# Kernel tuning notes

Hardware: AMD Instinct MI355X
Metric: run time of the kernel (lower is better)

## Reference

```python
import jax, jax.numpy as jnp
import numpy as np
import math

HIDDEN = 1024
N_HEADS = 16
N_KV = 4
HEAD_DIM = HIDDEN // N_HEADS  # 64
B, S = 2, 2048
THETA = 100000.0


def _freqs_cos_sin(dim, end, theta):
    # yarn params: original_max_position_embeddings=2048 >= end, so no ramp scaling,
    # attention_factor=1.0 -> plain RoPE frequencies.
    inv = 1.0 / theta ** (np.arange(0, dim, 2)[: dim // 2] / dim)
    t = np.arange(end)
    f = np.outer(t, inv).astype(np.float32)  # (end, dim/2)
    cos = np.concatenate([np.cos(f), np.cos(f)], axis=-1)  # (end, dim)
    sin = np.concatenate([np.sin(f), np.sin(f)], axis=-1)
    return jnp.asarray(cos), jnp.asarray(sin)


def _rotate(x):
    # stack([-x[...,1::2], x[...,::2]], -1).reshape_as(x)
    return jnp.stack([-x[..., 1::2], x[..., ::2]], axis=-1).reshape(x.shape)


def setup_inputs() -> dict:
    key = jax.random.key(0)
    ks = jax.random.split(key, 9)
    s = 0.02
    return {
        "hidden_states": jax.random.normal(ks[0], (B, S, HIDDEN), jnp.float32),
        "attention_mask": jnp.ones((B, S), jnp.int32),
        "Wq": jax.random.normal(ks[1], (HIDDEN, HIDDEN), jnp.float32) * s,
        "bq": jnp.zeros((HIDDEN,), jnp.float32),
        "Wk": jax.random.normal(ks[2], (HIDDEN, N_KV * HEAD_DIM), jnp.float32) * s,
        "bk": jnp.zeros((N_KV * HEAD_DIM,), jnp.float32),
        "Wv": jax.random.normal(ks[3], (HIDDEN, N_KV * HEAD_DIM), jnp.float32) * s,
        "bv": jnp.zeros((N_KV * HEAD_DIM,), jnp.float32),
        "Wo": jax.random.normal(ks[4], (HIDDEN, HIDDEN), jnp.float32) * s,
        "bo": jnp.zeros((HIDDEN,), jnp.float32),
    }


def reference(hidden_states, attention_mask, Wq, bq, Wk, bk, Wv, bv, Wo, bo):
    b, s, _ = hidden_states.shape
    q = (hidden_states @ Wq + bq).reshape(b, s, N_HEADS, HEAD_DIM)
    k = (hidden_states @ Wk + bk).reshape(b, s, N_KV, HEAD_DIM)
    v = (hidden_states @ Wv + bv).reshape(b, s, N_KV, HEAD_DIM)

    cos, sin = _freqs_cos_sin(HEAD_DIM, s, THETA)
    cos = cos[:, None, :]  # (s,1,d) broadcasts over (b,s,h,d)
    sin = sin[:, None, :]
    q = q * cos + _rotate(q) * sin
    k = k * cos + _rotate(k) * sin

    # GQA: repeat_interleave kv heads -> jnp.repeat along head axis
    rep = N_HEADS // N_KV
    k = jnp.repeat(k, rep, axis=2)
    v = jnp.repeat(v, rep, axis=2)

    scores = jnp.einsum("bqhd,bkhd->bhqk", q, k) / math.sqrt(HEAD_DIM)
    neg = jnp.finfo(scores.dtype).min
    causal = jnp.triu(jnp.ones((s, s), bool), k=1)  # (q,kv)
    bias = jnp.where(causal, neg, 0.0).astype(scores.dtype)[None, None]
    key_mask = attention_mask.astype(bool)[:, None, None, :]  # (b,1,1,kv)
    bias = jnp.where(key_mask, bias, neg)
    probs = jax.nn.softmax(scores + bias, axis=-1)
    attn = jnp.einsum("bhqk,bkhd->bqhd", probs, v).reshape(b, s, HIDDEN)
    return attn @ Wo + bo
```

## Files before the change

kernel.cpp:

```cpp
#include <hip/hip_runtime.h>
#include <cstddef>
#include <cstdint>

#define B_   2
#define S_   2048
#define HID  1024
#define NH_  16
#define NKV_ 4
#define DH_  64
#define ROWS (B_ * S_)
#define NQKV 1536
#define QSCALE 0.18033688011112042f

typedef __bf16 bf16_t;
typedef _Float16 f16_t;
typedef bf16_t bf16x8 __attribute__((ext_vector_type(8)));
typedef bf16_t bf16x4 __attribute__((ext_vector_type(4)));
typedef f16_t  f16x8  __attribute__((ext_vector_type(8)));
typedef f16_t  f16x4  __attribute__((ext_vector_type(4)));
typedef float  f32x4  __attribute__((ext_vector_type(4)));

typedef __attribute__((address_space(1))) const uint32_t gu32_t;
typedef __attribute__((address_space(3))) uint32_t lu32_t;

__device__ __forceinline__ void gl_lds16(const void* g, void* l) {
  __builtin_amdgcn_global_load_lds((gu32_t*)g, (lu32_t*)l, 16, 0, 0);
}

__global__ void prep_all(const float* __restrict__ hs,
                         const float* __restrict__ Wq, const float* __restrict__ Wk,
                         const float* __restrict__ Wv, const float* __restrict__ Wo,
                         const float* __restrict__ bq, const float* __restrict__ bk,
                         const float* __restrict__ bv,
                         bf16_t* __restrict__ hsb,
                         bf16_t* __restrict__ Wt, bf16_t* __restrict__ Wot,
                         float* __restrict__ ball, float2* __restrict__ lut)
{
  const int bid = blockIdx.x;
  if (bid < 2048) {
    const int i = (bid * 256 + threadIdx.x) * 8;
    float4 a = *(const float4*)(hs + i);
    float4 b = *(const float4*)(hs + i + 4);
    bf16x8 o;
    o[0]=(bf16_t)a.x; o[1]=(bf16_t)a.y; o[2]=(bf16_t)a.z; o[3]=(bf16_t)a.w;
    o[4]=(bf16_t)b.x; o[5]=(bf16_t)b.y; o[6]=(bf16_t)b.z; o[7]=(bf16_t)b.w;
    *(bf16x8*)(hsb + i) = o;
    return;
  }
  if (bid >= 4614) {
    const int idx = (bid - 4614) * 256 + threadIdx.x;
    const int s = idx >> 5, j = idx & 31;
    const float L = 0.51905126482615037f;
    const float ang = (float)s * exp2f(-L * (float)j);
    lut[idx] = make_float2(cosf(ang), sinf(ang));
    return;
  }
  if (bid >= 4608) {
    int i = (bid - 4608) * 256 + threadIdx.x;
    if (i < NQKV) ball[i] = (i < 1024) ? bq[i] : ((i < 1280) ? bk[i-1024] : bv[i-1280]);
    return;
  }
  const int wb = bid - 2048;
  const float* src; bf16_t* dst; int N, n0, k0;
  if (wb < 1024)      { src = Wq; dst = Wt;            N = 1024; int t = wb;      n0=(t&31)*32; k0=(t>>5)*32; }
  else if (wb < 1280) { src = Wk; dst = Wt + 1024*HID; N = 256;  int t = wb-1024; n0=(t&7)*32;  k0=(t>>3)*32; }
  else if (wb < 1536) { src = Wv; dst = Wt + 1280*HID; N = 256;  int t = wb-1280; n0=(t&7)*32;  k0=(t>>3)*32; }
  else                { src = Wo; dst = Wot;           N = 1024; int t = wb-1536; n0=(t&31)*32; k0=(t>>5)*32; }
  __shared__ bf16_t T[32][33];
  const int tx = threadIdx.x & 31, ty = threadIdx.x >> 5;
#pragma unroll
  for (int i = 0; i < 4; ++i)
    T[ty + i*8][tx] = (bf16_t)src[(size_t)(k0 + ty + i*8) * N + n0 + tx];
  __syncthreads();
#pragma unroll
  for (int i = 0; i < 4; ++i)
    dst[(size_t)(n0 + ty + i*8) * HID + k0 + tx] = T[tx][ty + i*8];
}

__global__ __launch_bounds__(512, 6) void gemm8w_b16o(
    const bf16_t* __restrict__ A, const bf16_t* __restrict__ Bt,
    const float* __restrict__ bias, bf16_t* __restrict__ C, int N)
{
  __shared__ bf16_t As[2][128 * 64];
  __shared__ bf16_t Bs[2][64 * 64];
  const int tid  = threadIdx.x;
  const int w    = tid >> 6;
  const int lane = tid & 63;
  const int m    = lane & 15;
  const int quad = lane >> 4;
  const int wm   = w >> 1;
  const int wn   = w & 1;
  const size_t bm = (size_t)blockIdx.y * 128;
  const size_t bn = (size_t)blockIdx.x * 64;

  const int sr   = lane >> 3;
  const int scol = (lane & 7) * 8;
  const bf16_t* Ag = A  + (bm + w * 16 + sr) * HID + scol;
  const bf16_t* Bg = Bt + (bn + w * 8  + sr) * HID + scol;

  f32x4 acc[2][2];
#pragma unroll
  for (int i = 0; i < 2; ++i)
#pragma unroll
    for (int j = 0; j < 2; ++j) acc[i][j] = (f32x4){0.f, 0.f, 0.f, 0.f};

  gl_lds16(Ag,            &As[0][(w * 16)     * 64]);
  gl_lds16(Ag + 8 * HID,  &As[0][(w * 16 + 8) * 64]);
  gl_lds16(Bg,            &Bs[0][(w * 8)      * 64]);

  int p = 0;
  for (int k0 = 0; k0 < HID; k0 += 64) {
    __syncthreads();
    if (k0 + 64 < HID) {
      gl_lds16(Ag + k0 + 64,           &As[p^1][(w * 16)     * 64]);
      gl_lds16(Ag + 8 * HID + k0 + 64, &As[p^1][(w * 16 + 8) * 64]);
      gl_lds16(Bg + k0 + 64,           &Bs[p^1][(w * 8)      * 64]);
    }
#pragma unroll
    for (int ks = 0; ks < 2; ++ks) {
      bf16x8 af[2], bfr[2];
#pragma unroll
      for (int mt = 0; mt < 2; ++mt)
        af[mt] = *(const bf16x8*)&As[p][(wm * 32 + mt * 16 + m) * 64 + ks * 32 + quad * 8];
#pragma unroll
      for (int nt = 0; nt < 2; ++nt)
        bfr[nt] = *(const bf16x8*)&Bs[p][(wn * 32 + nt * 16 + m) * 64 + ks * 32 + quad * 8];
#pragma unroll
      for (int mt = 0; mt < 2; ++mt)
#pragma unroll
        for (int nt = 0; nt < 2; ++nt)
          acc[mt][nt] = __builtin_amdgcn_mfma_f32_16x16x32_bf16(bfr[nt], af[mt], acc[mt][nt], 0, 0, 0);
    }
    p ^= 1;
  }
#pragma unroll
  for (int mt = 0; mt < 2; ++mt) {
    const size_t row = bm + wm * 32 + mt * 16 + m;
#pragma unroll
    for (int nt = 0; nt < 2; ++nt) {
      const size_t col = bn + wn * 32 + nt * 16 + quad * 4;
      float4 bb = *(const float4*)&bias[col];
      bf16x4 o;
      o[0] = (bf16_t)(acc[mt][nt][0] + bb.x);
      o[1] = (bf16_t)(acc[mt][nt][1] + bb.y);
      o[2] = (bf16_t)(acc[mt][nt][2] + bb.z);
      o[3] = (bf16_t)(acc[mt][nt][3] + bb.w);
      *(bf16x4*)&C[row * N + col] = o;
    }
  }
}

__global__ __launch_bounds__(256, 4) void gemm4w_f32o(
    const bf16_t* __restrict__ A, const bf16_t* __restrict__ Bt,
    const float* __restrict__ bias, float* __restrict__ C, int N)
{
  __shared__ bf16_t As[2][64 * 64];
  __shared__ bf16_t Bs[2][64 * 64];
  const int tid  = threadIdx.x;
  const int w    = tid >> 6;
  const int lane = tid & 63;
  const int m    = lane & 15;
  const int quad = lane >> 4;
  const int wm   = w >> 1;
  const int wn   = w & 1;
  const size_t bm = (size_t)blockIdx.y * 64;
  const size_t bn = (size_t)blockIdx.x * 64;

  const int sr   = lane >> 3;
  const int scol = (lane & 7) * 8;
  const bf16_t* Ag = A  + (bm + w * 16 + sr) * HID + scol;
  const bf16_t* Bg = Bt + (bn + w * 16 + sr) * HID + scol;

  f32x4 acc[2][2];
#pragma unroll
  for (int i = 0; i < 2; ++i)
#pragma unroll
    for (int j = 0; j < 2; ++j) acc[i][j] = (f32x4){0.f, 0.f, 0.f, 0.f};

  gl_lds16(Ag,           &As[0][(w * 16)     * 64]);
  gl_lds16(Ag + 8 * HID, &As[0][(w * 16 + 8) * 64]);
  gl_lds16(Bg,           &Bs[0][(w * 16)     * 64]);
  gl_lds16(Bg + 8 * HID, &Bs[0][(w * 16 + 8) * 64]);

  int p = 0;
  for (int k0 = 0; k0 < HID; k0 += 64) {
    __syncthreads();
    if (k0 + 64 < HID) {
      gl_lds16(Ag + k0 + 64,           &As[p^1][(w * 16)     * 64]);
      gl_lds16(Ag + 8 * HID + k0 + 64, &As[p^1][(w * 16 + 8) * 64]);
      gl_lds16(Bg + k0 + 64,           &Bs[p^1][(w * 16)     * 64]);
      gl_lds16(Bg + 8 * HID + k0 + 64, &Bs[p^1][(w * 16 + 8) * 64]);
    }
#pragma unroll
    for (int ks = 0; ks < 2; ++ks) {
      bf16x8 af[2], bfr[2];
#pragma unroll
      for (int mt = 0; mt < 2; ++mt)
        af[mt] = *(const bf16x8*)&As[p][(wm * 32 + mt * 16 + m) * 64 + ks * 32 + quad * 8];
#pragma unroll
      for (int nt = 0; nt < 2; ++nt)
        bfr[nt] = *(const bf16x8*)&Bs[p][(wn * 32 + nt * 16 + m) * 64 + ks * 32 + quad * 8];
#pragma unroll
      for (int mt = 0; mt < 2; ++mt)
#pragma unroll
        for (int nt = 0; nt < 2; ++nt)
          acc[mt][nt] = __builtin_amdgcn_mfma_f32_16x16x32_bf16(bfr[nt], af[mt], acc[mt][nt], 0, 0, 0);
    }
    p ^= 1;
  }
#pragma unroll
  for (int mt = 0; mt < 2; ++mt) {
    const size_t row = bm + wm * 32 + mt * 16 + m;
#pragma unroll
    for (int nt = 0; nt < 2; ++nt) {
      const size_t col = bn + wn * 32 + nt * 16 + quad * 4;
      float4 bb = *(const float4*)&bias[col];
      float4 o;
      o.x = acc[mt][nt][0] + bb.x; o.y = acc[mt][nt][1] + bb.y;
      o.z = acc[mt][nt][2] + bb.z; o.w = acc[mt][nt][3] + bb.w;
      *(float4*)&C[row * N + col] = o;
    }
  }
}

__global__ void prep_kv(const bf16_t* __restrict__ QKVb, const float2* __restrict__ lut,
                        bf16_t* __restrict__ Kimg, f16_t* __restrict__ Vimg)
{
  __shared__ bf16_t Lk[64][72];
  __shared__ bf16_t Lv[64][72];
  const int bid = blockIdx.x, t = threadIdx.x;
  const int kt = bid & 31, kvh = (bid >> 5) & 3, b = bid >> 7;
  const size_t img = ((size_t)(b * NKV_ + kvh) * 32 + kt) * 4096;

  {
    const int r0 = t >> 3, c8 = (t & 7) * 8;
#pragma unroll
    for (int i = 0; i < 2; ++i) {
      const int r = r0 + i * 32;
      const bf16_t* src = QKVb + (size_t)(b * S_ + kt * 64 + r) * NQKV + 1024 + kvh * DH_ + c8;
      *(bf16x8*)&Lk[r][c8] = *(const bf16x8*)src;
      *(bf16x8*)&Lv[r][c8] = *(const bf16x8*)(src + 256);
    }
  }
  __syncthreads();
  {
    const int key = t & 63, cg = t >> 6;
    const int srow = kt * 64 + key;
    bf16x8 a = *(const bf16x8*)&Lk[key][cg * 16];
    bf16x8 c = *(const bf16x8*)&Lk[key][cg * 16 + 8];
    const float2* lp = lut + srow * 32 + ((cg & 1) * 16);
    float v[16];
#pragma unroll
    for (int i = 0; i < 8; ++i) { v[i] = (float)a[i]; v[i + 8] = (float)c[i]; }
    bf16x8 o0, o1;
#pragma unroll
    for (int j = 0; j < 8; ++j) {
      const float2 ce = lp[2 * j], co = lp[2 * j + 1];
      const float y0 = v[2*j] * ce.x - v[2*j+1] * ce.y;
      const float y1 = v[2*j+1] * co.x + v[2*j] * co.y;
      if (j < 4) { o0[2*j] = (bf16_t)y0; o0[2*j+1] = (bf16_t)y1; }
      else       { o1[2*(j-4)] = (bf16_t)y0; o1[2*(j-4)+1] = (bf16_t)y1; }
    }
    const int s0 = (2 * cg) ^ (key & 7);
    *(bf16x8*)&Kimg[img + key * 64 + s0 * 8]       = o0;
    *(bf16x8*)&Kimg[img + key * 64 + (s0 ^ 1) * 8] = o1;
  }
  {
    const int d = t & 63, cg = t >> 6;
#pragma unroll
    for (int g4 = 0; g4 < 4; ++g4) {
      const int g = cg * 4 + g4;
      f16x4 o;
#pragma unroll
      for (int j = 0; j < 4; ++j)
        o[j] = (f16_t)(float)Lv[g * 4 + j][d];
      const int slot = g ^ (d & 15);
      *(f16x4*)&Vimg[img + d * 64 + slot * 4] = o;
    }
  }
}

#define PROC_TILE(AQ, OACC, LP, Q0W)                                          \
  do {                                                                        \
    f32x4 sc[4];                                                              \
    _Pragma("unroll") for (int cb = 0; cb < 4; ++cb)                          \
      sc[cb] = (f32x4){0.f, 0.f, 0.f, 0.f};                                   \
    _Pragma("unroll") for (int cb = 0; cb < 4; ++cb) {                        \
      const bf16x8 bk0 = *(const bf16x8*)&Ks[g][p][(cb*16 + m) * 64 + x0s * 8]; \
      const bf16x8 bk1 = *(const bf16x8*)&Ks[g][p][(cb*16 + m) * 64 + x1s * 8]; \
      sc[cb] = __builtin_amdgcn_mfma_f32_16x16x32_bf16(bk0, AQ[0], sc[cb], 0, 0, 0); \
      sc[cb] = __builtin_amdgcn_mfma_f32_16x16x32_bf16(bk1, AQ[1], sc[cb], 0, 0, 0); \
    }                                                                         \
    f16x4 bp[4];                                                              \
    {                                                                         \
      const bool needm = (kbase + 63 > (Q0W)) || (mb != ~0ull);               \
      if (needm) {                                                            \
        const int qv = (Q0W) + m;                                             \
        _Pragma("unroll") for (int cb = 0; cb < 4; ++cb)                      \
          _Pragma("unroll") for (int r = 0; r < 4; ++r) {                     \
            const int idx = cb*16 + quad*4 + r;                               \
            const bool ok = (kbase + idx <= qv) && ((mb >> idx) & 1);         \
            sc[cb][r] = ok ? sc[cb][r] : -1e38f;                              \
          }                                                                   \
      }                                                                       \
      float sum = 0.f;                                                        \
      _Pragma("unroll") for (int cb = 0; cb < 4; ++cb) {                      \
        f16x4 pp;                                                             \
        _Pragma("unroll") for (int r = 0; r < 4; ++r) {                       \
          const float pv = exp2f(sc[cb][r]);                                  \
          sum += pv;                                                          \
          pp[r] = (f16_t)pv;                                                  \
        }                                                                     \
        bp[cb] = pp;                                                          \
      }                                                                       \
      LP += sum;                                                              \
    }                                                                         \
    _Pragma("unroll") for (int cb = 0; cb < 4; ++cb) {                        \
      f16x4 av[4];                                                            \
      _Pragma("unroll") for (int dblk = 0; dblk < 4; ++dblk) {                \
        const int slot = (cb * 4 + quad) ^ m;                                 \
        av[dblk] = *(const f16x4*)&Vs[g][p][(dblk*16 + m) * 64 + slot * 4];   \
      }                                                                       \
      _Pragma("unroll") for (int dblk = 0; dblk < 4; ++dblk)                  \
        OACC[dblk] = __builtin_amdgcn_mfma_f32_16x16x16f16(av[dblk], bp[cb], OACC[dblk], 0, 0, 0); \
    }                                                                         \
  } while (0)

__global__ __launch_bounds__(512, 4) void attn_v8(
    const bf16_t* __restrict__ QKVb, const float2* __restrict__ lut,
    const bf16_t* __restrict__ Kt2, const f16_t* __restrict__ Vt2,
    const int* __restrict__ amask, bf16_t* __restrict__ Ab)
{
  __shared__ __align__(16) bf16_t Ks[2][2][64 * 64];
  __shared__ __align__(16) f16_t  Vs[2][2][64 * 64];

  const int tid  = threadIdx.x;
  const int w    = tid >> 6;
  const int g    = w >> 2;
  const int wl   = w & 3;
  const int lane = tid & 63;
  const int m    = lane & 15;
  const int quad = lane >> 4;
  const int kvh  = blockIdx.y;
  const int b    = blockIdx.z;
  const int h    = kvh * 4 + wl;
  const int x    = blockIdx.x;
  const int q0wA = x * 16;
  const int q0wB = (127 - x) * 16;
  const int nA   = (x >> 2) + 1;
  const int nB   = ((127 - x) >> 2) + 1;
  const int T    = nA + nB;

  bf16x8 aqA[2], aqB[2];
#pragma unroll
  for (int tt = 0; tt < 2; ++tt) {
    const int q0w_t = tt ? q0wB : q0wA;
    const int spos = q0w_t + m;
    const bf16_t* qsrc = QKVb + (size_t)(b * S_ + spos) * NQKV + h * DH_;
    float2 l8[8];
#pragma unroll
    for (int j = 0; j < 8; ++j) l8[j] = lut[spos * 32 + quad * 8 + j];
#pragma unroll
    for (int kc = 0; kc < 2; ++kc) {
      bf16x8 xv = *(const bf16x8*)(qsrc + kc * 32 + quad * 8);
      bf16x8 y;
#pragma unroll
      for (int i = 0; i < 4; ++i) {
        const float x0 = (float)xv[2*i], x1 = (float)xv[2*i+1];
        y[2*i]   = (bf16_t)((x0 * l8[2*i].x   - x1 * l8[2*i].y)   * QSCALE);
        y[2*i+1] = (bf16_t)((x1 * l8[2*i+1].x + x0 * l8[2*i+1].y) * QSCALE);
      }
      if (tt) aqB[kc] = y; else aqA[kc] = y;
    }
  }

  f32x4 oaccA[4], oaccB[4];
#pragma unroll
  for (int d = 0; d < 4; ++d) {
    oaccA[d] = (f32x4){0.f,0.f,0.f,0.f};
    oaccB[d] = (f32x4){0.f,0.f,0.f,0.f};
  }
  float lpA = 0.f, lpB = 0.f;

  const size_t imgbase = ((size_t)(b * NKV_ + kvh) * 32) * 4096;
  const bf16_t* Kg = Kt2 + imgbase;
  const f16_t*  Vg = Vt2 + imgbase;
  const int x0s = quad ^ (m & 7);
  const int x1s = (4 + quad) ^ (m & 7);
  const int* amp = amask + b * S_;

  int mcur;
  {
    const int e0  = g;
    const int kt0 = (e0 >= nA) ? e0 - nA : e0;
    const size_t off = (size_t)kt0 * 4096;
    gl_lds16(Kg + off + (2*wl)   * 512 + lane * 8, &Ks[g][0][(2*wl)   * 512]);
    gl_lds16(Kg + off + (2*wl+1) * 512 + lane * 8, &Ks[g][0][(2*wl+1) * 512]);
    gl_lds16(Vg + off + (2*wl)   * 512 + lane * 8, &Vs[g][0][(2*wl)   * 512]);
    gl_lds16(Vg + off + (2*wl+1) * 512 + lane * 8, &Vs[g][0][(2*wl+1) * 512]);
    mcur = amp[kt0 * 64 + lane];
  }

  int p = 0;
  const int niter = (T + 1) >> 1;
  for (int t = 0; t < niter; ++t) {
    const int e = 2 * t + g;
    __syncthreads();
    const int e2 = e + 2;
    const bool more = (e2 < T);
    int kt2 = 0;
    if (more) {
      kt2 = (e2 >= nA) ? e2 - nA : e2;
      const size_t off = (size_t)kt2 * 4096;
      gl_lds16(Kg + off + (2*wl)   * 512 + lane * 8, &Ks[g][p^1][(2*wl)   * 512]);
      gl_lds16(Kg + off + (2*wl+1) * 512 + lane * 8, &Ks[g][p^1][(2*wl+1) * 512]);
      gl_lds16(Vg + off + (2*wl)   * 512 + lane * 8, &Vs[g][p^1][(2*wl)   * 512]);
      gl_lds16(Vg + off + (2*wl+1) * 512 + lane * 8, &Vs[g][p^1][(2*wl+1) * 512]);
    }
    const int mnext = more ? amp[kt2 * 64 + lane] : 0;
    if (e < T) {
      const uint64_t mb = __ballot(mcur != 0);
      const bool isB = (e >= nA);
      const int kt = isB ? e - nA : e;
      const int kbase = kt * 64;
      if (isB) PROC_TILE(aqB, oaccB, lpB, q0wB);
      else     PROC_TILE(aqA, oaccA, lpA, q0wA);
    }
    mcur = mnext;
    p ^= 1;
  }

  float lAred = lpA;
  lAred += __shfl_xor(lAred, 16); lAred += __shfl_xor(lAred, 32);
  float lBred = lpB;
  lBred += __shfl_xor(lBred, 16); lBred += __shfl_xor(lBred, 32);

  __syncthreads();
  float* scrA = (float*)&Ks[0][0][0];
  float* scrB = (float*)&Vs[0][0][0];
  const int sbase = wl * 1104 + m * 68 + quad * 4;

  if (g == 0) {
#pragma unroll
    for (int dblk = 0; dblk < 4; ++dblk)
      *(f32x4*)&scrA[sbase + dblk * 16] = oaccA[dblk];
    if (quad == 0) scrA[wl * 1104 + 16 * 68 + m] = lAred;
  } else {
#pragma unroll
    for (int dblk = 0; dblk < 4; ++dblk)
      *(f32x4*)&scrB[sbase + dblk * 16] = oaccB[dblk];
    if (quad == 0) scrB[wl * 1104 + 16 * 68 + m] = lBred;
  }
  __syncthreads();

  if (g == 0) {
    const float l = lBred + scrB[wl * 1104 + 16 * 68 + m];
    const float inv = 1.0f / l;
    const size_t row = (size_t)(b * S_ + q0wB + m);
#pragma unroll
    for (int dblk = 0; dblk < 4; ++dblk) {
      const f32x4 part = *(const f32x4*)&scrB[sbase + dblk * 16];
      bf16x4 o;
      o[0] = (bf16_t)((oaccB[dblk][0] + part[0]) * inv);
      o[1] = (bf16_t)((oaccB[dblk][1] + part[1]) * inv);
      o[2] = (bf16_t)((oaccB[dblk][2] + part[2]) * inv);
      o[3] = (bf16_t)((oaccB[dblk][3] + part[3]) * inv);
      *(bf16x4*)&Ab[row * HID + h * DH_ + dblk * 16 + quad * 4] = o;
    }
  } else {
    const float l = lAred + scrA[wl * 1104 + 16 * 68 + m];
    const float inv = 1.0f / l;
    const size_t row = (size_t)(b * S_ + q0wA + m);
#pragma unroll
    for (int dblk = 0; dblk < 4; ++dblk) {
      const f32x4 part = *(const f32x4*)&scrA[sbase + dblk * 16];
      bf16x4 o;
      o[0] = (bf16_t)((oaccA[dblk][0] + part[0]) * inv);
      o[1] = (bf16_t)((oaccA[dblk][1] + part[1]) * inv);
      o[2] = (bf16_t)((oaccA[dblk][2] + part[2]) * inv);
      o[3] = (bf16_t)((oaccA[dblk][3] + part[3]) * inv);
      *(bf16x4*)&Ab[row * HID + h * DH_ + dblk * 16 + quad * 4] = o;
    }
  }
}

extern "C" void kernel_launch(void* const* d_in, const int* in_sizes, int n_in,
                              void* d_out, int out_size, void* d_ws, size_t ws_size,
                              hipStream_t stream)
{
  const float* hs    = (const float*)d_in[0];
  const int*   amask = (const int*)  d_in[1];
  const float* Wq    = (const float*)d_in[2];
  const float* bq    = (const float*)d_in[3];
  const float* Wk    = (const float*)d_in[4];
  const float* bk    = (const float*)d_in[5];
  const float* Wv    = (const float*)d_in[6];
  const float* bv    = (const float*)d_in[7];
  const float* Wo    = (const float*)d_in[8];
  const float* bo    = (const float*)d_in[9];
  float* out = (float*)d_out;

  bf16_t* QKVb = (bf16_t*)d_ws;
  bf16_t* hsb  = QKVb + (size_t)ROWS * NQKV;
  bf16_t* Wt   = hsb + (size_t)ROWS * HID;
  bf16_t* Wot  = Wt + (size_t)NQKV * HID;
  float*  ball = (float*)(Wot + (size_t)HID * HID);
  bf16_t* Kimg = (bf16_t*)(ball + NQKV);
  f16_t*  Vimg = (f16_t*)(Kimg + (size_t)B_*NKV_*32*4096);
  float2* lut  = (float2*)(Vimg + (size_t)B_*NKV_*32*4096);
  bf16_t* Ab   = hsb;

  prep_all<<<4870, 256, 0, stream>>>(hs, Wq, Wk, Wv, Wo, bq, bk, bv,
                                     hsb, Wt, Wot, ball, lut);

  gemm8w_b16o<<<dim3(NQKV/64, ROWS/128), 512, 0, stream>>>(hsb, Wt, ball, QKVb, NQKV);

  prep_kv<<<256, 256, 0, stream>>>(QKVb, lut, Kimg, Vimg);

  attn_v8<<<dim3(64, NKV_, B_), 512, 0, stream>>>(QKVb, lut, Kimg, Vimg, amask, Ab);

  gemm4w_f32o<<<dim3(HID/64, ROWS/64), 256, 0, stream>>>(Ab, Wot, bo, out, HID);
}
```

Baseline: 191.8 us.

## Triple-buffer both projection GEMMs with vmcnt waits and retile tiles

Both the QKV and output projection GEMMs move from double to triple-buffered LDS staging, prefetching two k-steps ahead. A single raw s_barrier is paired with explicit vmcnt waits, so later loads can stay in flight across the barrier. The QKV GEMM now uses 64x64 tiles with 4 waves instead of 128x64 with 8 waves. The output GEMM moves to 128x64 tiles, giving each wave more MFMA work per fragment load. The cost is more LDS per block and lower occupancy bounds. The hand-written waitcnt counts must match the per-thread load counts exactly, or the kernels will read stale tiles.

```diff
diff --git a/kernel.cpp b/kernel.cpp
--- a/kernel.cpp
+++ b/kernel.cpp
@@ -77,26 +77,33 @@
     dst[(size_t)(n0 + ty + i*8) * HID + k0 + tx] = T[tx][ty + i*8];
 }
 
-__global__ __launch_bounds__(512, 6) void gemm8w_b16o(
+#define STAGE_Q(buf, k0)                                                      \
+  do {                                                                        \
+    gl_lds16(Ag + (k0),           &As[buf][(w * 16)     * 64]);               \
+    gl_lds16(Ag + 8 * HID + (k0), &As[buf][(w * 16 + 8) * 64]);               \
+    gl_lds16(Bg + (k0),           &Bs[buf][(w * 16)     * 64]);               \
+    gl_lds16(Bg + 8 * HID + (k0), &Bs[buf][(w * 16 + 8) * 64]);               \
+  } while (0)
+
+__global__ __launch_bounds__(256, 3) void gemmQ(
     const bf16_t* __restrict__ A, const bf16_t* __restrict__ Bt,
     const float* __restrict__ bias, bf16_t* __restrict__ C, int N)
 {
-  __shared__ bf16_t As[2][128 * 64];
-  __shared__ bf16_t Bs[2][64 * 64];
+  __shared__ bf16_t As[3][64 * 64];
+  __shared__ bf16_t Bs[3][64 * 64];
   const int tid  = threadIdx.x;
   const int w    = tid >> 6;
   const int lane = tid & 63;
   const int m    = lane & 15;
   const int quad = lane >> 4;
-  const int wm   = w >> 1;
-  const int wn   = w & 1;
-  const size_t bm = (size_t)blockIdx.y * 128;
+  const int wm   = w >> 1, wn = w & 1;
+  const size_t bm = (size_t)blockIdx.y * 64;
   const size_t bn = (size_t)blockIdx.x * 64;
 
   const int sr   = lane >> 3;
   const int scol = (lane & 7) * 8;
   const bf16_t* Ag = A  + (bm + w * 16 + sr) * HID + scol;
-  const bf16_t* Bg = Bt + (bn + w * 8  + sr) * HID + scol;
+  const bf16_t* Bg = Bt + (bn + w * 16 + sr) * HID + scol;
 
   f32x4 acc[2][2];
 #pragma unroll
@@ -104,17 +111,19 @@
 #pragma unroll
     for (int j = 0; j < 2; ++j) acc[i][j] = (f32x4){0.f, 0.f, 0.f, 0.f};
 
-  gl_lds16(Ag,            &As[0][(w * 16)     * 64]);
-  gl_lds16(Ag + 8 * HID,  &As[0][(w * 16 + 8) * 64]);
-  gl_lds16(Bg,            &Bs[0][(w * 8)      * 64]);
+  STAGE_Q(0, 0);
+  STAGE_Q(1, 64);
 
   int p = 0;
-  for (int k0 = 0; k0 < HID; k0 += 64) {
-    __syncthreads();
-    if (k0 + 64 < HID) {
-      gl_lds16(Ag + k0 + 64,           &As[p^1][(w * 16)     * 64]);
-      gl_lds16(Ag + 8 * HID + k0 + 64, &As[p^1][(w * 16 + 8) * 64]);
-      gl_lds16(Bg + k0 + 64,           &Bs[p^1][(w * 8)      * 64]);
+  for (int t = 0; t < 16; ++t) {
+    if (t < 15) asm volatile("s_waitcnt vmcnt(4)" ::: "memory");
+    else        asm volatile("s_waitcnt vmcnt(0)" ::: "memory");
+    __builtin_amdgcn_sched_barrier(0);
+    __builtin_amdgcn_s_barrier();
+    __builtin_amdgcn_sched_barrier(0);
+    if (t + 2 < 16) {
+      const int pf = (p >= 1) ? p - 1 : 2;
+      STAGE_Q(pf, (t + 2) * 64);
     }
 #pragma unroll
     for (int ks = 0; ks < 2; ++ks) {
@@ -131,7 +140,7 @@
         for (int nt = 0; nt < 2; ++nt)
           acc[mt][nt] = __builtin_amdgcn_mfma_f32_16x16x32_bf16(bfr[nt], af[mt], acc[mt][nt], 0, 0, 0);
     }
-    p ^= 1;
+    p = (p < 2) ? p + 1 : 0;
   }
 #pragma unroll
   for (int mt = 0; mt < 2; ++mt) {
@@ -150,67 +159,76 @@
   }
 }
 
-__global__ __launch_bounds__(256, 4) void gemm4w_f32o(
+#define STAGE_O(buf, k0)                                                      \
+  do {                                                                        \
+    gl_lds16(Ag + (size_t)(0 * 32) * HID + (k0), &As[buf][(w * 8 + 0 * 32) * 64]); \
+    gl_lds16(Ag + (size_t)(1 * 32) * HID + (k0), &As[buf][(w * 8 + 1 * 32) * 64]); \
+    gl_lds16(Ag + (size_t)(2 * 32) * HID + (k0), &As[buf][(w * 8 + 2 * 32) * 64]); \
+    gl_lds16(Ag + (size_t)(3 * 32) * HID + (k0), &As[buf][(w * 8 + 3 * 32) * 64]); \
+    gl_lds16(Bg + (size_t)(0 * 32) * HID + (k0), &Bs[buf][(w * 8 + 0 * 32) * 64]); \
+    gl_lds16(Bg + (size_t)(1 * 32) * HID + (k0), &Bs[buf][(w * 8 + 1 * 32) * 64]); \
+  } while (0)
+
+__global__ __launch_bounds__(256, 2) void gemmO(
     const bf16_t* __restrict__ A, const bf16_t* __restrict__ Bt,
     const float* __restrict__ bias, float* __restrict__ C, int N)
 {
-  __shared__ bf16_t As[2][64 * 64];
-  __shared__ bf16_t Bs[2][64 * 64];
+  __shared__ bf16_t As[3][128 * 64];
+  __shared__ bf16_t Bs[3][64 * 64];
   const int tid  = threadIdx.x;
   const int w    = tid >> 6;
   const int lane = tid & 63;
   const int m    = lane & 15;
   const int quad = lane >> 4;
-  const int wm   = w >> 1;
-  const int wn   = w & 1;
-  const size_t bm = (size_t)blockIdx.y * 64;
+  const int wm   = w >> 1, wn = w & 1;
+  const size_t bm = (size_t)blockIdx.y * 128;
   const size_t bn = (size_t)blockIdx.x * 64;
 
-  const int sr   = lane >> 3;
+  const int srow = w * 8 + (lane >> 3);
   const int scol = (lane & 7) * 8;
-  const bf16_t* Ag = A  + (bm + w * 16 + sr) * HID + scol;
-  const bf16_t* Bg = Bt + (bn + w * 16 + sr) * HID + scol;
-
-  f32x4 acc[2][2];
-#pragma unroll
-  for (int i = 0; i < 2; ++i)
+  const bf16_t* Ag = A  + (bm + srow) * HID + scol;
+  const bf16_t* Bg = Bt + (bn + srow) * HID + scol;
+
+  f32x4 acc[4][2];
+#pragma unroll
+  for (int i = 0; i < 4; ++i)
 #pragma unroll
     for (int j = 0; j < 2; ++j) acc[i][j] = (f32x4){0.f, 0.f, 0.f, 0.f};
 
-  gl_lds16(Ag,           &As[0][(w * 16)     * 64]);
-  gl_lds16(Ag + 8 * HID, &As[0][(w * 16 + 8) * 64]);
-  gl_lds16(Bg,           &Bs[0][(w * 16)     * 64]);
-  gl_lds16(Bg + 8 * HID, &Bs[0][(w * 16 + 8) * 64]);
+  STAGE_O(0, 0);
+  STAGE_O(1, 64);
 
   int p = 0;
-  for (int k0 = 0; k0 < HID; k0 += 64) {
-    __syncthreads();
-    if (k0 + 64 < HID) {
-      gl_lds16(Ag + k0 + 64,           &As[p^1][(w * 16)     * 64]);
-      gl_lds16(Ag + 8 * HID + k0 + 64, &As[p^1][(w * 16 + 8) * 64]);
-      gl_lds16(Bg + k0 + 64,           &Bs[p^1][(w * 16)     * 64]);
-      gl_lds16(Bg + 8 * HID + k0 + 64, &Bs[p^1][(w * 16 + 8) * 64]);
+  for (int t = 0; t < 16; ++t) {
+    if (t < 15) asm volatile("s_waitcnt vmcnt(6)" ::: "memory");
+    else        asm volatile("s_waitcnt vmcnt(0)" ::: "memory");
+    __builtin_amdgcn_sched_barrier(0);
+    __builtin_amdgcn_s_barrier();
+    __builtin_amdgcn_sched_barrier(0);
+    if (t + 2 < 16) {
+      const int pf = (p >= 1) ? p - 1 : 2;
+      STAGE_O(pf, (t + 2) * 64);
     }
 #pragma unroll
     for (int ks = 0; ks < 2; ++ks) {
-      bf16x8 af[2], bfr[2];
-#pragma unroll
-      for (int mt = 0; mt < 2; ++mt)
-        af[mt] = *(const bf16x8*)&As[p][(wm * 32 + mt * 16 + m) * 64 + ks * 32 + quad * 8];
+      bf16x8 af[4], bfr[2];
+#pragma unroll
+      for (int mt = 0; mt < 4; ++mt)
+        af[mt] = *(const bf16x8*)&As[p][(wm * 64 + mt * 16 + m) * 64 + ks * 32 + quad * 8];
 #pragma unroll
       for (int nt = 0; nt < 2; ++nt)
         bfr[nt] = *(const bf16x8*)&Bs[p][(wn * 32 + nt * 16 + m) * 64 + ks * 32 + quad * 8];
 #pragma unroll
-      for (int mt = 0; mt < 2; ++mt)
+      for (int mt = 0; mt < 4; ++mt)
 #pragma unroll
         for (int nt = 0; nt < 2; ++nt)
           acc[mt][nt] = __builtin_amdgcn_mfma_f32_16x16x32_bf16(bfr[nt], af[mt], acc[mt][nt], 0, 0, 0);
     }
-    p ^= 1;
-  }
-#pragma unroll
-  for (int mt = 0; mt < 2; ++mt) {
-    const size_t row = bm + wm * 32 + mt * 16 + m;
+    p = (p < 2) ? p + 1 : 0;
+  }
+#pragma unroll
+  for (int mt = 0; mt < 4; ++mt) {
+    const size_t row = bm + wm * 64 + mt * 16 + m;
 #pragma unroll
     for (int nt = 0; nt < 2; ++nt) {
       const size_t col = bn + wn * 32 + nt * 16 + quad * 4;
@@ -513,11 +531,11 @@
   prep_all<<<4870, 256, 0, stream>>>(hs, Wq, Wk, Wv, Wo, bq, bk, bv,
                                      hsb, Wt, Wot, ball, lut);
 
-  gemm8w_b16o<<<dim3(NQKV/64, ROWS/128), 512, 0, stream>>>(hsb, Wt, ball, QKVb, NQKV);
+  gemmQ<<<dim3(NQKV/64, ROWS/64), 256, 0, stream>>>(hsb, Wt, ball, QKVb, NQKV);
 
   prep_kv<<<256, 256, 0, stream>>>(QKVb, lut, Kimg, Vimg);
 
   attn_v8<<<dim3(64, NKV_, B_), 512, 0, stream>>>(QKVb, lut, Kimg, Vimg, amask, Ab);
 
-  gemm4w_f32o<<<dim3(HID/64, ROWS/64), 256, 0, stream>>>(Ab, Wot, bo, out, HID);
-}
+  gemmO<<<dim3(HID/64, ROWS/128), 256, 0, stream>>>(Ab, Wot, bo, out, HID);
+}
```

After: 194.3 us. Within noise of the previous version (+1.3%).
